# Optimization experiments

Measured on AMD Instinct MI355X. Metric: run time of the kernel, lower is better.

The kernel has to match this reference:

```python
import jax, jax.numpy as jnp
import numpy as np

B, S, D = 4, 2048, 1024
E, K, H = 8, 2, 2816


def setup_inputs() -> dict:
    key = jax.random.key(0)
    ks = jax.random.split(key, 5)
    x = jax.random.normal(ks[0], (B, S, D), dtype=jnp.float32)
    gate_w = jax.random.normal(ks[1], (E, D), dtype=jnp.float32) * (D ** -0.5)
    w1 = jax.random.normal(ks[2], (E, D, H), dtype=jnp.float32) * (D ** -0.5)
    w2 = jax.random.normal(ks[3], (E, H, D), dtype=jnp.float32) * (H ** -0.5)
    w3 = jax.random.normal(ks[4], (E, D, H), dtype=jnp.float32) * (D ** -0.5)
    return {"x": x, "gate_w": gate_w, "w1": w1, "w2": w2, "w3": w3}


def reference(x, gate_w, w1, w2, w3):
    b, s, d = x.shape
    T = b * s
    xf = x.reshape(T, d)
    # Router: scores -> top-k -> softmax over the k selected scores
    scores = xf @ gate_w.T                      # [T, E]
    top_w, top_idx = jax.lax.top_k(scores, K)   # [T, K]
    top_w = jax.nn.softmax(top_w, axis=-1)      # softmax over the k experts
    # Combine weights scattered into a dense [T, E] matrix (each row has K nonzeros)
    combine = jnp.zeros((T, E), dtype=x.dtype).at[
        jnp.arange(T)[:, None], top_idx
    ].add(top_w)                                # [T, E]
    # Per-expert SwiGLU MLP, weighted combine (fixed small loop over experts)
    out = jnp.zeros((T, d), dtype=x.dtype)
    for e in range(E):
        h = jax.nn.silu(xf @ w1[e]) * (xf @ w3[e])   # [T, H]
        out = out + combine[:, e:e + 1] * (h @ w2[e])
    return out.reshape(b, s, d)
```

## Files before the change

### kernel.cpp

```cpp
#include <hip/hip_runtime.h>
#include <math.h>

#define T_TOK 8192
#define DIM   1024
#define HID   2816
#define NE    8

typedef __attribute__((ext_vector_type(4))) float  f32x4;
typedef __attribute__((ext_vector_type(8))) __bf16 bf16x8;
typedef __attribute__((ext_vector_type(8))) unsigned short u16x8;

__device__ __forceinline__ unsigned short f2bf(float f) {
  unsigned int u = __builtin_bit_cast(unsigned int, f);
  unsigned int r = (u + 0x7FFFu + ((u >> 16) & 1u)) >> 16;
  return (unsigned short)r;
}
__device__ __forceinline__ int imin(int a, int b) { return a < b ? a : b; }

typedef const __attribute__((address_space(1))) void gvoid_t;
typedef __attribute__((address_space(3))) void svoid_t;
__device__ __forceinline__ void g2l16(const void* g, void* l) {
  __builtin_amdgcn_global_load_lds((gvoid_t*)g, (svoid_t*)l, 16, 0, 0);
}

#define WAITV(N) asm volatile("s_waitcnt vmcnt(" #N ")" ::: "memory")
#define WAITV0 asm volatile("s_waitcnt vmcnt(0)" ::: "memory")
#define LGKM0  asm volatile("s_waitcnt lgkmcnt(0)" ::: "memory")
#define FENCE  asm volatile("" ::: "memory")
#define SBAR   __builtin_amdgcn_s_barrier()
#define SCHED0 __builtin_amdgcn_sched_barrier(0)
#define PRIO(x) __builtin_amdgcn_s_setprio(x)
#define PH_PRE  do { FENCE; SBAR; LGKM0; SCHED0; PRIO(1); } while (0)
#define PH_POST do { PRIO(0); FENCE; SBAR; SCHED0; } while (0)

#define NT1 (HID / 128)
#define NT2 (DIM / 256)
#define TPM ((DIM / 64) * (HID / 64) * NE)
#define RTB (T_TOK / 4)
#define TBLK ((3 * TPM) / 2)
#define LDSTR 65

__global__ __launch_bounds__(256) void front_kernel(const float* __restrict__ x,
                                                    const float* __restrict__ gw,
                                                    const float* __restrict__ w1,
                                                    const float* __restrict__ w3,
                                                    const float* __restrict__ w2,
                                                    unsigned short* __restrict__ xb,
                                                    unsigned short* __restrict__ w1t,
                                                    unsigned short* __restrict__ w3t,
                                                    unsigned short* __restrict__ w2t,
                                                    int* __restrict__ choice,
                                                    float* __restrict__ wslot) {
  __shared__ float lds[64 * LDSTR];
  int bid = blockIdx.x;
  if (bid < RTB) {
    int wid = threadIdx.x >> 6;
    int lane = threadIdx.x & 63;
    int t = bid * 4 + wid;
    double acc[NE];
#pragma unroll
    for (int e = 0; e < NE; ++e) acc[e] = 0.0;
    const float* xr = x + (size_t)t * DIM;
    unsigned short* xbr = xb + (size_t)t * DIM;
#pragma unroll 4
    for (int i = 0; i < DIM / 64; ++i) {
      int d = i * 64 + lane;
      float xf = xr[d];
      xbr[d] = f2bf(xf);
      double xv = (double)xf;
#pragma unroll
      for (int e = 0; e < NE; ++e) acc[e] += xv * (double)gw[e * DIM + d];
    }
#pragma unroll
    for (int e = 0; e < NE; ++e) {
#pragma unroll
      for (int off = 32; off >= 1; off >>= 1) acc[e] += __shfl_xor(acc[e], off);
    }
    if (lane == 0) {
      int e0 = 0; double s0 = acc[0];
#pragma unroll
      for (int e = 1; e < NE; ++e) if (acc[e] > s0) { s0 = acc[e]; e0 = e; }
      int e1 = -1; double s1 = -1.0e300;
#pragma unroll
      for (int e = 0; e < NE; ++e) if (e != e0 && acc[e] > s1) { s1 = acc[e]; e1 = e; }
      double w0 = 1.0 / (1.0 + exp(s1 - s0));
      wslot[t] = (float)w0;
      wslot[T_TOK + t] = (float)(1.0 - w0);
      choice[t] = e0 | (e1 << 4);
    }
    return;
  }

  int tb = bid - RTB;
  const int tr = threadIdx.x >> 4;
  const int tc4 = (threadIdx.x & 15) * 4;
  const int cw = threadIdx.x >> 3;
  const int r8 = (threadIdx.x & 7) * 8;

  const float* sA; unsigned short* dA; int cA, RA;
  const float* sB; unsigned short* dB; int cB, RB;
#pragma unroll
  for (int tau = 0; tau < 2; ++tau) {
    int g = tb * 2 + tau;
    int seg = g / TPM, rr = g % TPM;
    const float* srcm; unsigned short* dstm; int R, C;
    if (seg == 0)      { srcm = w1; dstm = w1t; R = DIM; C = HID; }
    else if (seg == 1) { srcm = w3; dstm = w3t; R = DIM; C = HID; }
    else               { srcm = w2; dstm = w2t; R = HID; C = DIM; }
    int per_e = (R / 64) * (C / 64);
    int e = rr / per_e, tt = rr % per_e;
    int nx = C / 64;
    int c0 = (tt % nx) * 64, r0 = (tt / nx) * 64;
    const float* s = srcm + (size_t)e * R * C + (size_t)(r0 + tr) * C + c0 + tc4;
    unsigned short* d = dstm + (size_t)e * R * C + (size_t)c0 * R + r0;
    if (tau == 0) { sA = s; dA = d; cA = C; RA = R; }
    else          { sB = s; dB = d; cB = C; RB = R; }
  }

  float4 v0[4], v1[4];
#pragma unroll
  for (int s4 = 0; s4 < 4; ++s4)
    v0[s4] = *(const float4*)(sA + (size_t)(s4 * 16) * cA);
#pragma unroll
  for (int s4 = 0; s4 < 4; ++s4) {
    float* lr = &lds[(tr + s4 * 16) * LDSTR + tc4];
    lr[0] = v0[s4].x; lr[1] = v0[s4].y; lr[2] = v0[s4].z; lr[3] = v0[s4].w;
  }
  __syncthreads();
#pragma unroll
  for (int s4 = 0; s4 < 4; ++s4)
    v1[s4] = *(const float4*)(sB + (size_t)(s4 * 16) * cB);
#pragma unroll
  for (int pass = 0; pass < 2; ++pass) {
    int c = cw + pass * 32;
    u16x8 o;
#pragma unroll
    for (int k = 0; k < 8; ++k) o[k] = f2bf(lds[(r8 + k) * LDSTR + c]);
    *(u16x8*)(dA + (size_t)c * RA + r8) = o;
  }
  __syncthreads();
#pragma unroll
  for (int s4 = 0; s4 < 4; ++s4) {
    float* lr = &lds[(tr + s4 * 16) * LDSTR + tc4];
    lr[0] = v1[s4].x; lr[1] = v1[s4].y; lr[2] = v1[s4].z; lr[3] = v1[s4].w;
  }
  __syncthreads();
#pragma unroll
  for (int pass = 0; pass < 2; ++pass) {
    int c = cw + pass * 32;
    u16x8 o;
#pragma unroll
    for (int k = 0; k < 8; ++k) o[k] = f2bf(lds[(r8 + k) * LDSTR + c]);
    *(u16x8*)(dB + (size_t)c * RB + r8) = o;
  }
}

__global__ __launch_bounds__(1024) void compact_kernel(const int* __restrict__ choice,
                                                       int* __restrict__ cnt,
                                                       int* __restrict__ idx) {
  int e = blockIdx.x;
  __shared__ int wsum[16], wbase[16], blkbase;
  if (threadIdx.x == 0) blkbase = 0;
  __syncthreads();
  int lane = threadIdx.x & 63, wv = threadIdx.x >> 6;
  int* out = idx + e * T_TOK;
#pragma unroll 1
  for (int chunk = 0; chunk < T_TOK; chunk += 1024) {
    int t = chunk + threadIdx.x;
    int ch = choice[t];
    int ent = -1;
    if ((ch & 15) == e) ent = t;
    else if (((ch >> 4) & 15) == e) ent = t | (1 << 15);
    unsigned long long mask = __ballot(ent >= 0);
    int mypos = __popcll(mask & ((1ull << lane) - 1ull));
    if (lane == 0) wsum[wv] = __popcll(mask);
    __syncthreads();
    if (threadIdx.x == 0) {
      int s = blkbase;
#pragma unroll
      for (int i = 0; i < 16; ++i) { wbase[i] = s; s += wsum[i]; }
      blkbase = s;
    }
    __syncthreads();
    if (ent >= 0) out[wbase[wv] + mypos] = ent;
    __syncthreads();
  }
  if (threadIdx.x == 0) cnt[e] = blkbase;
}

__device__ __forceinline__ bool decode_tile(const int* __restrict__ cnt, int ntiles_n,
                                            int nscale, int& e, int& n0, int& m0,
                                            int& c, int& base) {
  int nt = 0;
#pragma unroll
  for (int i = 0; i < NE; ++i) nt += ((cnt[i] + 255) >> 8) * ntiles_n;
  int q = nt >> 3, rr = nt & 7;
  int xcd = blockIdx.x & 7, pos = blockIdx.x >> 3;
  int cap = xcd < rr ? q + 1 : q;
  if (pos >= cap) return false;
  int lid = (xcd < rr ? xcd * (q + 1) : rr * (q + 1) + (xcd - rr) * q) + pos;
  int t1 = 0, s = 0;
  e = 0; c = 0; base = 0; n0 = 0; m0 = 0;
#pragma unroll
  for (int i = 0; i < NE; ++i) {
    int ci = cnt[i];
    int mi = (ci + 255) >> 8;
    int w = mi * ntiles_n;
    if (lid >= t1 && lid < t1 + w) {
      e = i; c = ci; base = s;
      int rem = lid - t1;
      int n = rem / mi;
      n0 = n * nscale;
      m0 = (rem - n * mi) * 256;
    }
    t1 += w; s += ci;
  }
  return true;
}

__global__ __launch_bounds__(512, 1) void gemm1_kernel(const unsigned short* __restrict__ xb,
                                                       const unsigned short* __restrict__ w1t,
                                                       const unsigned short* __restrict__ w3t,
                                                       const int* __restrict__ cnt,
                                                       const int* __restrict__ idx,
                                                       unsigned short* __restrict__ hbuf) {
  int e, n0, m0, c, base;
  if (!decode_tile(cnt, NT1, 128, e, n0, m0, c, base)) return;

  __shared__ __align__(16) unsigned short As[2 * 16384];
  __shared__ __align__(16) unsigned short B1s[2 * 8192];
  __shared__ __align__(16) unsigned short B3s[2 * 8192];

  const int t = threadIdx.x;
  const int wid = t >> 6, lane = t & 63;
  const int wm = wid >> 2, wn = wid & 3;
  const int lr = lane & 15, kc = lane >> 4, sw = lane & 7;
  const int ldst = wid * 512;
  const int trow = t >> 3;
  const int swzk = ((t & 7) ^ ((t >> 3) & 7)) * 8;

  const int* idx_e = idx + e * T_TOK;
  int g0 = m0 + trow, g1 = m0 + 64 + trow, g2 = m0 + 128 + trow, g3 = m0 + 192 + trow;
  int tk0 = (g0 < c) ? (idx_e[g0] & 0x1FFF) : 0;
  int tk1 = (g1 < c) ? (idx_e[g1] & 0x1FFF) : 0;
  int tk2 = (g2 < c) ? (idx_e[g2] & 0x1FFF) : 0;
  int tk3 = (g3 < c) ? (idx_e[g3] & 0x1FFF) : 0;
  const unsigned short* aS0 = xb + (size_t)tk0 * DIM + swzk;
  const unsigned short* aS1 = xb + (size_t)tk1 * DIM + swzk;
  const unsigned short* aS2 = xb + (size_t)tk2 * DIM + swzk;
  const unsigned short* aS3 = xb + (size_t)tk3 * DIM + swzk;
  const unsigned short* w1e = w1t + ((size_t)e * HID + n0) * DIM;
  const unsigned short* w3e = w3t + ((size_t)e * HID + n0) * DIM;
  const unsigned short* b1S0 = w1e + (size_t)trow * DIM + swzk;
  const unsigned short* b1S1 = w1e + (size_t)(64 + trow) * DIM + swzk;
  const unsigned short* b3S0 = w3e + (size_t)trow * DIM + swzk;
  const unsigned short* b3S1 = w3e + (size_t)(64 + trow) * DIM + swzk;

  f32x4 acc1[8][2], acc3[8][2];
#pragma unroll
  for (int i = 0; i < 8; ++i)
#pragma unroll
    for (int j = 0; j < 2; ++j) {
      acc1[i][j] = f32x4{0.f, 0.f, 0.f, 0.f};
      acc3[i][j] = f32x4{0.f, 0.f, 0.f, 0.f};
    }
  bf16x8 ra0[4], ra1[4], rb1[2], rb3[2];

#define G1_STG_A(CUR, TILE) do {                                      \
    g2l16(aS0 + (TILE) * 64, As + (CUR) * 16384 + 0 * 4096 + ldst);   \
    g2l16(aS1 + (TILE) * 64, As + (CUR) * 16384 + 1 * 4096 + ldst);   \
    g2l16(aS2 + (TILE) * 64, As + (CUR) * 16384 + 2 * 4096 + ldst);   \
    g2l16(aS3 + (TILE) * 64, As + (CUR) * 16384 + 3 * 4096 + ldst);   \
  } while (0)
#define G1_STG_B(CUR, TILE) do {                                      \
    g2l16(b1S0 + (TILE) * 64, B1s + (CUR) * 8192 + 0 * 4096 + ldst);  \
    g2l16(b1S1 + (TILE) * 64, B1s + (CUR) * 8192 + 1 * 4096 + ldst);  \
    g2l16(b3S0 + (TILE) * 64, B3s + (CUR) * 8192 + 0 * 4096 + ldst);  \
    g2l16(b3S1 + (TILE) * 64, B3s + (CUR) * 8192 + 1 * 4096 + ldst);  \
  } while (0)
#define G1_LDALL(CUR, KS2) do {                                                        \
    const int se = ((((KS2) * 4) + kc) ^ sw) * 8;                                      \
    rb1[0] = *(const bf16x8*)(B1s + (CUR) * 8192 + (wn * 32 + lr) * 64 + se);          \
    rb1[1] = *(const bf16x8*)(B1s + (CUR) * 8192 + (wn * 32 + 16 + lr) * 64 + se);     \
    rb3[0] = *(const bf16x8*)(B3s + (CUR) * 8192 + (wn * 32 + lr) * 64 + se);          \
    rb3[1] = *(const bf16x8*)(B3s + (CUR) * 8192 + (wn * 32 + 16 + lr) * 64 + se);     \
    const int ab = (CUR) * 16384 + (wm * 128 + lr) * 64 + se;                          \
    _Pragma("unroll") for (int f = 0; f < 4; ++f) {                                    \
      ra0[f] = *(const bf16x8*)(As + ab + f * 1024);                                   \
      ra1[f] = *(const bf16x8*)(As + ab + 4096 + f * 1024);                            \
    }                                                                                  \
  } while (0)
#define G1_MM2() do {                                                                  \
    _Pragma("unroll") for (int f = 0; f < 4; ++f)                                      \
      _Pragma("unroll") for (int j = 0; j < 2; ++j) {                                  \
        acc1[f][j] = __builtin_amdgcn_mfma_f32_16x16x32_bf16(ra0[f], rb1[j], acc1[f][j], 0, 0, 0); \
        acc3[f][j] = __builtin_amdgcn_mfma_f32_16x16x32_bf16(ra0[f], rb3[j], acc3[f][j], 0, 0, 0); \
      }                                                                                \
    _Pragma("unroll") for (int f = 0; f < 4; ++f)                                      \
      _Pragma("unroll") for (int j = 0; j < 2; ++j) {                                  \
        acc1[4 + f][j] = __builtin_amdgcn_mfma_f32_16x16x32_bf16(ra1[f], rb1[j], acc1[4 + f][j], 0, 0, 0); \
        acc3[4 + f][j] = __builtin_amdgcn_mfma_f32_16x16x32_bf16(ra1[f], rb3[j], acc3[4 + f][j], 0, 0, 0); \
      }                                                                                \
  } while (0)
#define G1_ITER(CUR, KT, DOSTAGE) do {                                                 \
    G1_LDALL(CUR, 0);                                                                  \
    PH_PRE; G1_MM2(); PH_POST;                                                         \
    G1_LDALL(CUR, 1);                                                                  \
    FENCE; SBAR; LGKM0; SCHED0; PRIO(1); G1_MM2(); PRIO(0); SCHED0;                    \
    if (DOSTAGE) { G1_STG_A(CUR, (KT) + 2); G1_STG_B(CUR, (KT) + 2); WAITV(8); }       \
    else WAITV0;                                                                       \
    FENCE; SBAR; SCHED0;                                                               \
  } while (0)

  G1_STG_A(0, 0); G1_STG_B(0, 0);
  G1_STG_A(1, 1); G1_STG_B(1, 1);
  WAITV(8); FENCE; SBAR; SCHED0;

  const int NK = DIM / 64;
#pragma unroll 1
  for (int kt = 0; kt < NK; kt += 2) {
    G1_ITER(0, kt, (kt + 2) < NK);
    G1_ITER(1, kt + 1, (kt + 3) < NK);
  }

#pragma unroll
  for (int i = 0; i < 8; ++i)
#pragma unroll
    for (int q = 0; q < 4; ++q) {
      int pl = m0 + wm * 128 + i * 16 + kc * 4 + q;
      if (pl >= c) continue;
      unsigned short* hrow = hbuf + (size_t)(base + pl) * HID + n0 + wn * 32 + lr;
#pragma unroll
      for (int j = 0; j < 2; ++j) {
        float v1 = acc1[i][j][q];
        float v3 = acc3[i][j][q];
        float hv = v1 / (1.0f + __expf(-v1)) * v3;
        hrow[j * 16] = f2bf(hv);
      }
    }
}

__global__ __launch_bounds__(512, 1) void gemm2_kernel(const unsigned short* __restrict__ hbuf,
                                                       const unsigned short* __restrict__ w2t,
                                                       const int* __restrict__ cnt,
                                                       const int* __restrict__ idx,
                                                       const float* __restrict__ wslot,
                                                       float* __restrict__ part0,
                                                       float* __restrict__ part1) {
  int e, n0, m0, c, base;
  if (!decode_tile(cnt, NT2, 256, e, n0, m0, c, base)) return;

  __shared__ __align__(16) unsigned short As[2 * 16384];
  __shared__ __align__(16) unsigned short Bs[2 * 16384];

  const int t = threadIdx.x;
  const int wid = t >> 6, lane = t & 63;
  const int wm = wid >> 1, wn = wid & 1;
  const int lr = lane & 15, kc = lane >> 4, sw = lane & 7;
  const int ldst = wid * 512;
  const int trow = t >> 3;
  const int swzk = ((t & 7) ^ ((t >> 3) & 7)) * 8;

  int r0 = imin(base + m0 + trow,       2 * T_TOK - 1);
  int r1 = imin(base + m0 + 64 + trow,  2 * T_TOK - 1);
  int r2 = imin(base + m0 + 128 + trow, 2 * T_TOK - 1);
  int r3 = imin(base + m0 + 192 + trow, 2 * T_TOK - 1);
  const unsigned short* aS0 = hbuf + (size_t)r0 * HID + swzk;
  const unsigned short* aS1 = hbuf + (size_t)r1 * HID + swzk;
  const unsigned short* aS2 = hbuf + (size_t)r2 * HID + swzk;
  const unsigned short* aS3 = hbuf + (size_t)r3 * HID + swzk;
  const unsigned short* w2e = w2t + ((size_t)e * DIM + n0) * HID;
  const unsigned short* bS0 = w2e + (size_t)trow * HID + swzk;
  const unsigned short* bS1 = w2e + (size_t)(64 + trow) * HID + swzk;
  const unsigned short* bS2 = w2e + (size_t)(128 + trow) * HID + swzk;
  const unsigned short* bS3 = w2e + (size_t)(192 + trow) * HID + swzk;

  f32x4 acc[4][8];
#pragma unroll
  for (int i = 0; i < 4; ++i)
#pragma unroll
    for (int j = 0; j < 8; ++j) acc[i][j] = f32x4{0.f, 0.f, 0.f, 0.f};
  bf16x8 ra[4], rb[8];

#define G2_STG(CUR, TILE) do {                                        \
    g2l16(aS0 + (TILE) * 64, As + (CUR) * 16384 + 0 * 4096 + ldst);   \
    g2l16(aS1 + (TILE) * 64, As + (CUR) * 16384 + 1 * 4096 + ldst);   \
    g2l16(aS2 + (TILE) * 64, As + (CUR) * 16384 + 2 * 4096 + ldst);   \
    g2l16(aS3 + (TILE) * 64, As + (CUR) * 16384 + 3 * 4096 + ldst);   \
    g2l16(bS0 + (TILE) * 64, Bs + (CUR) * 16384 + 0 * 4096 + ldst);   \
    g2l16(bS1 + (TILE) * 64, Bs + (CUR) * 16384 + 1 * 4096 + ldst);   \
    g2l16(bS2 + (TILE) * 64, Bs + (CUR) * 16384 + 2 * 4096 + ldst);   \
    g2l16(bS3 + (TILE) * 64, Bs + (CUR) * 16384 + 3 * 4096 + ldst);   \
  } while (0)
#define G2_LD(CUR, KS2) do {                                                          \
    const int se = ((((KS2) * 4) + kc) ^ sw) * 8;                                     \
    const int ab = (CUR) * 16384 + (wm * 64 + lr) * 64 + se;                          \
    _Pragma("unroll") for (int f = 0; f < 4; ++f)                                     \
      ra[f] = *(const bf16x8*)(As + ab + f * 1024);                                   \
    const int bb = (CUR) * 16384 + (wn * 128 + lr) * 64 + se;                         \
    _Pragma("unroll") for (int j = 0; j < 8; ++j)                                     \
      rb[j] = *(const bf16x8*)(Bs + bb + j * 1024);                                   \
  } while (0)
#define G2_MM() do {                                                                  \
    _Pragma("unroll") for (int f = 0; f < 4; ++f)                                     \
      _Pragma("unroll") for (int j = 0; j < 8; ++j)                                   \
        acc[f][j] = __builtin_amdgcn_mfma_f32_16x16x32_bf16(ra[f], rb[j], acc[f][j], 0, 0, 0); \
  } while (0)
#define G2_ITER(CUR, KT, DOSTAGE) do {                                                \
    G2_LD(CUR, 0);                                                                    \
    PH_PRE; G2_MM(); PH_POST;                                                         \
    G2_LD(CUR, 1);                                                                    \
    FENCE; SBAR; LGKM0; SCHED0; PRIO(1); G2_MM(); PRIO(0); SCHED0;                    \
    if (DOSTAGE) { G2_STG(CUR, (KT) + 2); WAITV(8); }                                 \
    else WAITV0;                                                                      \
    FENCE; SBAR; SCHED0;                                                              \
  } while (0)

  G2_STG(0, 0);
  G2_STG(1, 1);
  WAITV(8); FENCE; SBAR; SCHED0;

  const int NK = HID / 64;
#pragma unroll 1
  for (int kt = 0; kt < NK; kt += 2) {
    G2_ITER(0, kt, (kt + 2) < NK);
    G2_ITER(1, kt + 1, (kt + 3) < NK);
  }

  const int* idx_e = idx + e * T_TOK;
#pragma unroll
  for (int i = 0; i < 4; ++i)
#pragma unroll
    for (int q = 0; q < 4; ++q) {
      int pl = m0 + wm * 64 + i * 16 + kc * 4 + q;
      if (pl >= c) continue;
      int ent = idx_e[pl];
      int tok = ent & 0x1FFF;
      int slot = (ent >> 15) & 1;
      float w = wslot[slot * T_TOK + tok];
      float* pp = slot ? part1 : part0;
      float* orow = pp + (size_t)tok * DIM + n0 + wn * 128 + lr;
#pragma unroll
      for (int j = 0; j < 8; ++j)
        orow[j * 16] = w * acc[i][j][q];
    }
}

__global__ __launch_bounds__(256) void combine_kernel(const float* __restrict__ p0,
                                                      const float* __restrict__ p1,
                                                      float* __restrict__ out) {
  int i = blockIdx.x * 256 + threadIdx.x;
  float4 a = ((const float4*)p0)[i];
  float4 b = ((const float4*)p1)[i];
  float4 o;
  o.x = a.x + b.x;
  o.y = a.y + b.y;
  o.z = a.z + b.z;
  o.w = a.w + b.w;
  ((float4*)out)[i] = o;
}

extern "C" void kernel_launch(void* const* d_in, const int* in_sizes, int n_in,
                              void* d_out, int out_size, void* d_ws, size_t ws_size,
                              hipStream_t stream) {
  const float* x  = (const float*)d_in[0];
  const float* gw = (const float*)d_in[1];
  const float* w1 = (const float*)d_in[2];
  const float* w2 = (const float*)d_in[3];
  const float* w3 = (const float*)d_in[4];
  float* out = (float*)d_out;

  char* ws = (char*)d_ws;
  size_t off = 0;
  auto alloc = [&](size_t bytes) {
    char* p = ws + off;
    off += (bytes + 255) & ~(size_t)255;
    return p;
  };
  unsigned short* xb  = (unsigned short*)alloc((size_t)T_TOK * DIM * 2);
  unsigned short* w1t = (unsigned short*)alloc((size_t)NE * DIM * HID * 2);
  unsigned short* w3t = (unsigned short*)alloc((size_t)NE * DIM * HID * 2);
  unsigned short* w2t = (unsigned short*)alloc((size_t)NE * DIM * HID * 2);
  unsigned short* hb  = (unsigned short*)alloc((size_t)2 * T_TOK * HID * 2);
  int*   cnt    = (int*)alloc(NE * sizeof(int));
  int*   choice = (int*)alloc((size_t)T_TOK * sizeof(int));
  int*   idx    = (int*)alloc((size_t)NE * T_TOK * sizeof(int));
  float* wslot  = (float*)alloc((size_t)2 * T_TOK * sizeof(float));
  float* part0 = (float*)w1t;
  float* part1 = part0 + (size_t)T_TOK * DIM;

  front_kernel<<<RTB + TBLK, 256, 0, stream>>>(x, gw, w1, w3, w2, xb,
                                               w1t, w3t, w2t, choice, wslot);
  compact_kernel<<<NE, 1024, 0, stream>>>(choice, cnt, idx);
  gemm1_kernel<<<72 * NT1, 512, 0, stream>>>(xb, w1t, w3t, cnt, idx, hb);
  gemm2_kernel<<<72 * NT2, 512, 0, stream>>>(hb, w2t, cnt, idx, wslot, part0, part1);
  combine_kernel<<<(T_TOK * DIM) / (4 * 256), 256, 0, stream>>>(part0, part1, out);
}
```

Baseline: 530.0 us.

## Halve K tile to 32 in both expert GEMMs to fit two blocks per CU

Both grouped GEMM kernels change their K tile from 64 to 32, halving shared-memory buffers (64KB to 32KB) and relaxing launch bounds from (512,1) to (512), so two workgroups may co-reside per CU. The LDS swizzle, staging addressing and per-iteration phasing are rewritten to match, with one compute phase per tile instead of two sub-steps. This trades more barriers and K iterations for higher occupancy and latency hiding, but register pressure from the large accumulator arrays may still prevent a second block.

```diff
diff --git a/kernel.cpp b/kernel.cpp
--- a/kernel.cpp
+++ b/kernel.cpp
@@ -30,8 +30,6 @@
 #define SBAR   __builtin_amdgcn_s_barrier()
 #define SCHED0 __builtin_amdgcn_sched_barrier(0)
 #define PRIO(x) __builtin_amdgcn_s_setprio(x)
-#define PH_PRE  do { FENCE; SBAR; LGKM0; SCHED0; PRIO(1); } while (0)
-#define PH_POST do { PRIO(0); FENCE; SBAR; SCHED0; } while (0)
 
 #define NT1 (HID / 128)
 #define NT2 (DIM / 256)
@@ -218,43 +216,38 @@
   return true;
 }
 
-__global__ __launch_bounds__(512, 1) void gemm1_kernel(const unsigned short* __restrict__ xb,
-                                                       const unsigned short* __restrict__ w1t,
-                                                       const unsigned short* __restrict__ w3t,
-                                                       const int* __restrict__ cnt,
-                                                       const int* __restrict__ idx,
-                                                       unsigned short* __restrict__ hbuf) {
+__global__ __launch_bounds__(512) void gemm1_kernel(const unsigned short* __restrict__ xb,
+                                                    const unsigned short* __restrict__ w1t,
+                                                    const unsigned short* __restrict__ w3t,
+                                                    const int* __restrict__ cnt,
+                                                    const int* __restrict__ idx,
+                                                    unsigned short* __restrict__ hbuf) {
   int e, n0, m0, c, base;
   if (!decode_tile(cnt, NT1, 128, e, n0, m0, c, base)) return;
 
-  __shared__ __align__(16) unsigned short As[2 * 16384];
-  __shared__ __align__(16) unsigned short B1s[2 * 8192];
-  __shared__ __align__(16) unsigned short B3s[2 * 8192];
+  __shared__ __align__(16) unsigned short As[2 * 8192];
+  __shared__ __align__(16) unsigned short B1s[2 * 4096];
+  __shared__ __align__(16) unsigned short B3s[2 * 4096];
 
   const int t = threadIdx.x;
   const int wid = t >> 6, lane = t & 63;
   const int wm = wid >> 2, wn = wid & 3;
-  const int lr = lane & 15, kc = lane >> 4, sw = lane & 7;
+  const int lr = lane & 15, kc = lane >> 4;
   const int ldst = wid * 512;
-  const int trow = t >> 3;
-  const int swzk = ((t & 7) ^ ((t >> 3) & 7)) * 8;
+  const int trow = t >> 2;
+  const int swzk = ((t & 3) ^ ((t >> 3) & 3)) * 8;
+  const int se = (kc ^ ((lane >> 1) & 3)) * 8;
 
   const int* idx_e = idx + e * T_TOK;
-  int g0 = m0 + trow, g1 = m0 + 64 + trow, g2 = m0 + 128 + trow, g3 = m0 + 192 + trow;
+  int g0 = m0 + trow, g1 = m0 + 128 + trow;
   int tk0 = (g0 < c) ? (idx_e[g0] & 0x1FFF) : 0;
   int tk1 = (g1 < c) ? (idx_e[g1] & 0x1FFF) : 0;
-  int tk2 = (g2 < c) ? (idx_e[g2] & 0x1FFF) : 0;
-  int tk3 = (g3 < c) ? (idx_e[g3] & 0x1FFF) : 0;
   const unsigned short* aS0 = xb + (size_t)tk0 * DIM + swzk;
   const unsigned short* aS1 = xb + (size_t)tk1 * DIM + swzk;
-  const unsigned short* aS2 = xb + (size_t)tk2 * DIM + swzk;
-  const unsigned short* aS3 = xb + (size_t)tk3 * DIM + swzk;
   const unsigned short* w1e = w1t + ((size_t)e * HID + n0) * DIM;
   const unsigned short* w3e = w3t + ((size_t)e * HID + n0) * DIM;
   const unsigned short* b1S0 = w1e + (size_t)trow * DIM + swzk;
-  const unsigned short* b1S1 = w1e + (size_t)(64 + trow) * DIM + swzk;
   const unsigned short* b3S0 = w3e + (size_t)trow * DIM + swzk;
-  const unsigned short* b3S1 = w3e + (size_t)(64 + trow) * DIM + swzk;
 
   f32x4 acc1[8][2], acc3[8][2];
 #pragma unroll
@@ -264,59 +257,43 @@
       acc1[i][j] = f32x4{0.f, 0.f, 0.f, 0.f};
       acc3[i][j] = f32x4{0.f, 0.f, 0.f, 0.f};
     }
-  bf16x8 ra0[4], ra1[4], rb1[2], rb3[2];
-
-#define G1_STG_A(CUR, TILE) do {                                      \
-    g2l16(aS0 + (TILE) * 64, As + (CUR) * 16384 + 0 * 4096 + ldst);   \
-    g2l16(aS1 + (TILE) * 64, As + (CUR) * 16384 + 1 * 4096 + ldst);   \
-    g2l16(aS2 + (TILE) * 64, As + (CUR) * 16384 + 2 * 4096 + ldst);   \
-    g2l16(aS3 + (TILE) * 64, As + (CUR) * 16384 + 3 * 4096 + ldst);   \
-  } while (0)
-#define G1_STG_B(CUR, TILE) do {                                      \
-    g2l16(b1S0 + (TILE) * 64, B1s + (CUR) * 8192 + 0 * 4096 + ldst);  \
-    g2l16(b1S1 + (TILE) * 64, B1s + (CUR) * 8192 + 1 * 4096 + ldst);  \
-    g2l16(b3S0 + (TILE) * 64, B3s + (CUR) * 8192 + 0 * 4096 + ldst);  \
-    g2l16(b3S1 + (TILE) * 64, B3s + (CUR) * 8192 + 1 * 4096 + ldst);  \
-  } while (0)
-#define G1_LDALL(CUR, KS2) do {                                                        \
-    const int se = ((((KS2) * 4) + kc) ^ sw) * 8;                                      \
-    rb1[0] = *(const bf16x8*)(B1s + (CUR) * 8192 + (wn * 32 + lr) * 64 + se);          \
-    rb1[1] = *(const bf16x8*)(B1s + (CUR) * 8192 + (wn * 32 + 16 + lr) * 64 + se);     \
-    rb3[0] = *(const bf16x8*)(B3s + (CUR) * 8192 + (wn * 32 + lr) * 64 + se);          \
-    rb3[1] = *(const bf16x8*)(B3s + (CUR) * 8192 + (wn * 32 + 16 + lr) * 64 + se);     \
-    const int ab = (CUR) * 16384 + (wm * 128 + lr) * 64 + se;                          \
-    _Pragma("unroll") for (int f = 0; f < 4; ++f) {                                    \
-      ra0[f] = *(const bf16x8*)(As + ab + f * 1024);                                   \
-      ra1[f] = *(const bf16x8*)(As + ab + 4096 + f * 1024);                            \
-    }                                                                                  \
-  } while (0)
-#define G1_MM2() do {                                                                  \
-    _Pragma("unroll") for (int f = 0; f < 4; ++f)                                      \
+  bf16x8 ra[8], rb1[2], rb3[2];
+
+#define G1_STG(CUR, TILE) do {                                        \
+    g2l16(aS0 + (TILE) * 32, As + (CUR) * 8192 + ldst);               \
+    g2l16(aS1 + (TILE) * 32, As + (CUR) * 8192 + 4096 + ldst);        \
+    g2l16(b1S0 + (TILE) * 32, B1s + (CUR) * 4096 + ldst);             \
+    g2l16(b3S0 + (TILE) * 32, B3s + (CUR) * 4096 + ldst);             \
+  } while (0)
+#define G1_LDALL(CUR) do {                                                             \
+    rb1[0] = *(const bf16x8*)(B1s + (CUR) * 4096 + (wn * 32 + lr) * 32 + se);          \
+    rb1[1] = *(const bf16x8*)(B1s + (CUR) * 4096 + (wn * 32 + 16 + lr) * 32 + se);     \
+    rb3[0] = *(const bf16x8*)(B3s + (CUR) * 4096 + (wn * 32 + lr) * 32 + se);          \
+    rb3[1] = *(const bf16x8*)(B3s + (CUR) * 4096 + (wn * 32 + 16 + lr) * 32 + se);     \
+    _Pragma("unroll") for (int f = 0; f < 8; ++f)                                      \
+      ra[f] = *(const bf16x8*)(As + (CUR) * 8192 + (wm * 128 + f * 16 + lr) * 32 + se);\
+  } while (0)
+#define G1_MM() do {                                                                   \
+    _Pragma("unroll") for (int f = 0; f < 8; ++f)                                      \
       _Pragma("unroll") for (int j = 0; j < 2; ++j) {                                  \
-        acc1[f][j] = __builtin_amdgcn_mfma_f32_16x16x32_bf16(ra0[f], rb1[j], acc1[f][j], 0, 0, 0); \
-        acc3[f][j] = __builtin_amdgcn_mfma_f32_16x16x32_bf16(ra0[f], rb3[j], acc3[f][j], 0, 0, 0); \
+        acc1[f][j] = __builtin_amdgcn_mfma_f32_16x16x32_bf16(ra[f], rb1[j], acc1[f][j], 0, 0, 0); \
+        acc3[f][j] = __builtin_amdgcn_mfma_f32_16x16x32_bf16(ra[f], rb3[j], acc3[f][j], 0, 0, 0); \
       }                                                                                \
-    _Pragma("unroll") for (int f = 0; f < 4; ++f)                                      \
-      _Pragma("unroll") for (int j = 0; j < 2; ++j) {                                  \
-        acc1[4 + f][j] = __builtin_amdgcn_mfma_f32_16x16x32_bf16(ra1[f], rb1[j], acc1[4 + f][j], 0, 0, 0); \
-        acc3[4 + f][j] = __builtin_amdgcn_mfma_f32_16x16x32_bf16(ra1[f], rb3[j], acc3[4 + f][j], 0, 0, 0); \
-      }                                                                                \
   } while (0)
 #define G1_ITER(CUR, KT, DOSTAGE) do {                                                 \
-    G1_LDALL(CUR, 0);                                                                  \
-    PH_PRE; G1_MM2(); PH_POST;                                                         \
-    G1_LDALL(CUR, 1);                                                                  \
-    FENCE; SBAR; LGKM0; SCHED0; PRIO(1); G1_MM2(); PRIO(0); SCHED0;                    \
-    if (DOSTAGE) { G1_STG_A(CUR, (KT) + 2); G1_STG_B(CUR, (KT) + 2); WAITV(8); }       \
+    G1_LDALL(CUR);                                                                     \
+    LGKM0; FENCE; SBAR; SCHED0;                                                        \
+    PRIO(1); G1_MM(); PRIO(0); SCHED0;                                                 \
+    if (DOSTAGE) { G1_STG(CUR, (KT) + 2); WAITV(4); }                                  \
     else WAITV0;                                                                       \
     FENCE; SBAR; SCHED0;                                                               \
   } while (0)
 
-  G1_STG_A(0, 0); G1_STG_B(0, 0);
-  G1_STG_A(1, 1); G1_STG_B(1, 1);
-  WAITV(8); FENCE; SBAR; SCHED0;
-
-  const int NK = DIM / 64;
+  G1_STG(0, 0);
+  G1_STG(1, 1);
+  WAITV(4); FENCE; SBAR; SCHED0;
+
+  const int NK = DIM / 32;
 #pragma unroll 1
   for (int kt = 0; kt < NK; kt += 2) {
     G1_ITER(0, kt, (kt + 2) < NK);
@@ -340,40 +317,35 @@
     }
 }
 
-__global__ __launch_bounds__(512, 1) void gemm2_kernel(const unsigned short* __restrict__ hbuf,
-                                                       const unsigned short* __restrict__ w2t,
-                                                       const int* __restrict__ cnt,
-                                                       const int* __restrict__ idx,
-                                                       const float* __restrict__ wslot,
-                                                       float* __restrict__ part0,
-                                                       float* __restrict__ part1) {
+__global__ __launch_bounds__(512) void gemm2_kernel(const unsigned short* __restrict__ hbuf,
+                                                    const unsigned short* __restrict__ w2t,
+                                                    const int* __restrict__ cnt,
+                                                    const int* __restrict__ idx,
+                                                    const float* __restrict__ wslot,
+                                                    float* __restrict__ part0,
+                                                    float* __restrict__ part1) {
   int e, n0, m0, c, base;
   if (!decode_tile(cnt, NT2, 256, e, n0, m0, c, base)) return;
 
-  __shared__ __align__(16) unsigned short As[2 * 16384];
-  __shared__ __align__(16) unsigned short Bs[2 * 16384];
+  __shared__ __align__(16) unsigned short As[2 * 8192];
+  __shared__ __align__(16) unsigned short Bs[2 * 8192];
 
   const int t = threadIdx.x;
   const int wid = t >> 6, lane = t & 63;
   const int wm = wid >> 1, wn = wid & 1;
-  const int lr = lane & 15, kc = lane >> 4, sw = lane & 7;
+  const int lr = lane & 15, kc = lane >> 4;
   const int ldst = wid * 512;
-  const int trow = t >> 3;
-  const int swzk = ((t & 7) ^ ((t >> 3) & 7)) * 8;
+  const int trow = t >> 2;
+  const int swzk = ((t & 3) ^ ((t >> 3) & 3)) * 8;
+  const int se = (kc ^ ((lane >> 1) & 3)) * 8;
 
   int r0 = imin(base + m0 + trow,       2 * T_TOK - 1);
-  int r1 = imin(base + m0 + 64 + trow,  2 * T_TOK - 1);
-  int r2 = imin(base + m0 + 128 + trow, 2 * T_TOK - 1);
-  int r3 = imin(base + m0 + 192 + trow, 2 * T_TOK - 1);
+  int r1 = imin(base + m0 + 128 + trow, 2 * T_TOK - 1);
   const unsigned short* aS0 = hbuf + (size_t)r0 * HID + swzk;
   const unsigned short* aS1 = hbuf + (size_t)r1 * HID + swzk;
-  const unsigned short* aS2 = hbuf + (size_t)r2 * HID + swzk;
-  const unsigned short* aS3 = hbuf + (size_t)r3 * HID + swzk;
   const unsigned short* w2e = w2t + ((size_t)e * DIM + n0) * HID;
   const unsigned short* bS0 = w2e + (size_t)trow * HID + swzk;
-  const unsigned short* bS1 = w2e + (size_t)(64 + trow) * HID + swzk;
-  const unsigned short* bS2 = w2e + (size_t)(128 + trow) * HID + swzk;
-  const unsigned short* bS3 = w2e + (size_t)(192 + trow) * HID + swzk;
+  const unsigned short* bS1 = w2e + (size_t)(128 + trow) * HID + swzk;
 
   f32x4 acc[4][8];
 #pragma unroll
@@ -383,44 +355,36 @@
   bf16x8 ra[4], rb[8];
 
 #define G2_STG(CUR, TILE) do {                                        \
-    g2l16(aS0 + (TILE) * 64, As + (CUR) * 16384 + 0 * 4096 + ldst);   \
-    g2l16(aS1 + (TILE) * 64, As + (CUR) * 16384 + 1 * 4096 + ldst);   \
-    g2l16(aS2 + (TILE) * 64, As + (CUR) * 16384 + 2 * 4096 + ldst);   \
-    g2l16(aS3 + (TILE) * 64, As + (CUR) * 16384 + 3 * 4096 + ldst);   \
-    g2l16(bS0 + (TILE) * 64, Bs + (CUR) * 16384 + 0 * 4096 + ldst);   \
-    g2l16(bS1 + (TILE) * 64, Bs + (CUR) * 16384 + 1 * 4096 + ldst);   \
-    g2l16(bS2 + (TILE) * 64, Bs + (CUR) * 16384 + 2 * 4096 + ldst);   \
-    g2l16(bS3 + (TILE) * 64, Bs + (CUR) * 16384 + 3 * 4096 + ldst);   \
-  } while (0)
-#define G2_LD(CUR, KS2) do {                                                          \
-    const int se = ((((KS2) * 4) + kc) ^ sw) * 8;                                     \
-    const int ab = (CUR) * 16384 + (wm * 64 + lr) * 64 + se;                          \
-    _Pragma("unroll") for (int f = 0; f < 4; ++f)                                     \
-      ra[f] = *(const bf16x8*)(As + ab + f * 1024);                                   \
-    const int bb = (CUR) * 16384 + (wn * 128 + lr) * 64 + se;                         \
-    _Pragma("unroll") for (int j = 0; j < 8; ++j)                                     \
-      rb[j] = *(const bf16x8*)(Bs + bb + j * 1024);                                   \
-  } while (0)
-#define G2_MM() do {                                                                  \
-    _Pragma("unroll") for (int f = 0; f < 4; ++f)                                     \
-      _Pragma("unroll") for (int j = 0; j < 8; ++j)                                   \
+    g2l16(aS0 + (TILE) * 32, As + (CUR) * 8192 + ldst);               \
+    g2l16(aS1 + (TILE) * 32, As + (CUR) * 8192 + 4096 + ldst);        \
+    g2l16(bS0 + (TILE) * 32, Bs + (CUR) * 8192 + ldst);               \
+    g2l16(bS1 + (TILE) * 32, Bs + (CUR) * 8192 + 4096 + ldst);        \
+  } while (0)
+#define G2_LDALL(CUR) do {                                                             \
+    _Pragma("unroll") for (int f = 0; f < 4; ++f)                                      \
+      ra[f] = *(const bf16x8*)(As + (CUR) * 8192 + (wm * 64 + f * 16 + lr) * 32 + se); \
+    _Pragma("unroll") for (int j = 0; j < 8; ++j)                                      \
+      rb[j] = *(const bf16x8*)(Bs + (CUR) * 8192 + (wn * 128 + j * 16 + lr) * 32 + se);\
+  } while (0)
+#define G2_MM() do {                                                                   \
+    _Pragma("unroll") for (int f = 0; f < 4; ++f)                                      \
+      _Pragma("unroll") for (int j = 0; j < 8; ++j)                                    \
         acc[f][j] = __builtin_amdgcn_mfma_f32_16x16x32_bf16(ra[f], rb[j], acc[f][j], 0, 0, 0); \
   } while (0)
-#define G2_ITER(CUR, KT, DOSTAGE) do {                                                \
-    G2_LD(CUR, 0);                                                                    \
-    PH_PRE; G2_MM(); PH_POST;                                                         \
-    G2_LD(CUR, 1);                                                                    \
-    FENCE; SBAR; LGKM0; SCHED0; PRIO(1); G2_MM(); PRIO(0); SCHED0;                    \
-    if (DOSTAGE) { G2_STG(CUR, (KT) + 2); WAITV(8); }                                 \
-    else WAITV0;                                                                      \
-    FENCE; SBAR; SCHED0;                                                              \
+#define G2_ITER(CUR, KT, DOSTAGE) do {                                                 \
+    G2_LDALL(CUR);                                                                     \
+    LGKM0; FENCE; SBAR; SCHED0;                                                        \
+    PRIO(1); G2_MM(); PRIO(0); SCHED0;                                                 \
+    if (DOSTAGE) { G2_STG(CUR, (KT) + 2); WAITV(4); }                                  \
+    else WAITV0;                                                                       \
+    FENCE; SBAR; SCHED0;                                                               \
   } while (0)
 
   G2_STG(0, 0);
   G2_STG(1, 1);
-  WAITV(8); FENCE; SBAR; SCHED0;
-
-  const int NK = HID / 64;
+  WAITV(4); FENCE; SBAR; SCHED0;
+
+  const int NK = HID / 32;
 #pragma unroll 1
   for (int kt = 0; kt < NK; kt += 2) {
     G2_ITER(0, kt, (kt + 2) < NK);
```

New measurement: 585.9 us. +10.5%, slower.
